# Optimization experiments

Hardware: AMD Instinct MI355X
Metric: run time of the kernel (lower is better)

## Reference

```python
import jax, jax.numpy as jnp
import numpy as np

N = 100000
E = 1600000
IN_C = 128
HID = 128
EMB = 64
EPS = 1e-5


def setup_inputs() -> dict:
    key = jax.random.key(0)
    ks = jax.random.split(key, 8)
    x = jax.random.normal(ks[0], (N, IN_C), dtype=jnp.float32)
    edge_index = jax.random.randint(ks[1], (2, E), 0, N, dtype=jnp.int64)
    s1 = 1.0 / np.sqrt(IN_C)
    s2 = 1.0 / np.sqrt(HID)
    # SAGEConv layer 1: lin_l (aggregated neighbors, with bias), lin_r (root, no bias)
    W1l = jax.random.uniform(ks[2], (IN_C, HID), jnp.float32, -s1, s1)
    b1 = jnp.zeros((HID,), jnp.float32)
    W1r = jax.random.uniform(ks[3], (IN_C, HID), jnp.float32, -s1, s1)
    g1 = jnp.ones((HID,), jnp.float32)
    be1 = jnp.zeros((HID,), jnp.float32)
    # SAGEConv layer 2
    W2l = jax.random.uniform(ks[4], (HID, EMB), jnp.float32, -s2, s2)
    b2 = jnp.zeros((EMB,), jnp.float32)
    W2r = jax.random.uniform(ks[5], (HID, EMB), jnp.float32, -s2, s2)
    g2 = jnp.ones((EMB,), jnp.float32)
    be2 = jnp.zeros((EMB,), jnp.float32)
    return {"x": x, "edge_index": edge_index,
            "W1l": W1l, "b1": b1, "W1r": W1r, "g1": g1, "be1": be1,
            "W2l": W2l, "b2": b2, "W2r": W2r, "g2": g2, "be2": be2}


def _mean_aggregate(x, src, dst, n_nodes):
    # mean of source-node features over incoming edges at each dst node
    msg_sum = jax.ops.segment_sum(x[src], dst, num_segments=n_nodes)  # [N, C]
    cnt = jax.ops.segment_sum(jnp.ones((src.shape[0],), x.dtype), dst,
                              num_segments=n_nodes)
    return msg_sum / jnp.maximum(cnt, 1.0)[:, None]


def _sage_conv(x, src, dst, Wl, b, Wr):
    agg = _mean_aggregate(x, src, dst, x.shape[0])
    return agg @ Wl + b + x @ Wr


def _batch_norm_eval(x, gamma, beta):
    # eval-mode BN with running_mean=0, running_var=1
    return x * (gamma / jnp.sqrt(1.0 + EPS)) + beta


def reference(x, edge_index, W1l, b1, W1r, g1, be1, W2l, b2, W2r, g2, be2):
    src, dst = edge_index[0], edge_index[1]
    h = _sage_conv(x, src, dst, W1l, b1, W1r)
    h = jax.nn.relu(_batch_norm_eval(h, g1, be1))  # dropout is identity in eval
    h = _sage_conv(h, src, dst, W2l, b2, W2r)
    h = jax.nn.relu(_batch_norm_eval(h, g2, be2))
    return h
```

## Files before the change

kernel.cpp:

```cpp
#include <hip/hip_runtime.h>
#include <math.h>

#define EPS 1e-5f
#define BSH 9
#define BSPAN 512
#define CHUNK 2048
#define CAP 16384

typedef __attribute__((ext_vector_type(8))) short short8;
typedef __attribute__((ext_vector_type(4))) float f32x4;

__device__ __forceinline__ short f2bf(float f) {
  union { float f; unsigned u; } v; v.f = f;
  unsigned r = v.u + 0x7fff + ((v.u >> 16) & 1);
  return (short)(r >> 16);
}
__device__ __forceinline__ float bf2f(unsigned short u) {
  union { unsigned u; float f; } v; v.u = ((unsigned)u) << 16; return v.f;
}

__global__ __launch_bounds__(256) void k_prep(
    const float* __restrict__ x, unsigned short* __restrict__ xbf, long long n8,
    const int* __restrict__ ei, int* __restrict__ bcnt, int E, int n,
    int ncast, int nhist,
    const float* __restrict__ W1l, const float* __restrict__ W1r,
    short* __restrict__ wp1,
    const float* __restrict__ W2l, const float* __restrict__ W2r,
    short* __restrict__ wp2) {
  __shared__ int h[256];
  int b = blockIdx.x, tid = threadIdx.x;
  if (b < ncast) {
    long long i = (long long)b * 256 + tid;
    if (i < n8) {
      const float4* p = (const float4*)x + i * 2;
      float4 v0 = p[0], v1 = p[1];
      short8 o;
      o[0] = f2bf(v0.x); o[1] = f2bf(v0.y); o[2] = f2bf(v0.z); o[3] = f2bf(v0.w);
      o[4] = f2bf(v1.x); o[5] = f2bf(v1.y); o[6] = f2bf(v1.z); o[7] = f2bf(v1.w);
      ((short8*)xbf)[i] = o;
    }
  } else if (b < ncast + nhist) {
    h[tid] = 0;
    __syncthreads();
    long long base = (long long)(b - ncast) * CHUNK;
#pragma unroll
    for (int i = 0; i < CHUNK / 256; ++i) {
      long long e = base + i * 256 + tid;
      if (e < E) {
        int d = ei[E + e];
        if ((unsigned)d < (unsigned)n) atomicAdd(&h[d >> BSH], 1);
      }
    }
    __syncthreads();
    if (h[tid]) atomicAdd(&bcnt[tid], h[tid]);
  } else if (b < ncast + nhist + 16) {
    int t = (b - ncast - nhist) * 256 + tid;
    int l = t & 63, f = t >> 6;
    int kt = f >> 3, ct = f & 7;
    int c = ct * 16 + (l & 15);
    int kb = kt * 32 + (l >> 4) * 8;
    short8 v;
#pragma unroll
    for (int j = 0; j < 8; ++j) {
      int k = kb + j;
      float w = (k < 128) ? W1l[k * 128 + c] : W1r[(k - 128) * 128 + c];
      v[j] = f2bf(w);
    }
    *(short8*)(wp1 + (size_t)t * 8) = v;
  } else {
    int t = (b - ncast - nhist - 16) * 256 + tid;
    int l = t & 63, f = t >> 6;
    int kt = f >> 3, ct = f & 7;
    int c = ct * 16 + (l & 15);
    int kb = kt * 32 + (l >> 4) * 8;
    short8 v;
#pragma unroll
    for (int j = 0; j < 8; ++j) {
      int k = kb + j;
      float w = (c < 64) ? W2l[k * 64 + c] : W2r[k * 64 + (c - 64)];
      v[j] = f2bf(w);
    }
    *(short8*)(wp2 + (size_t)t * 8) = v;
  }
}

__global__ __launch_bounds__(256) void k_bscan(
    const int* __restrict__ bcnt, int* __restrict__ bbase,
    int* __restrict__ bcur, int nbk) {
  __shared__ int s[256];
  int t = threadIdx.x;
  int v = (t < nbk) ? bcnt[t] : 0;
  s[t] = v;
  __syncthreads();
  for (int off = 1; off < 256; off <<= 1) {
    int xv = (t >= off) ? s[t - off] : 0;
    __syncthreads();
    s[t] += xv;
    __syncthreads();
  }
  int excl = s[t] - v;
  if (t < nbk) { bbase[t] = excl; bcur[t] = excl; }
}

__global__ __launch_bounds__(256) void k_scatter(
    const int* __restrict__ ei, int* __restrict__ bcur,
    unsigned* __restrict__ epk, int E, int n) {
  __shared__ int h[256];
  __shared__ int base[256];
  int tid = threadIdx.x;
  h[tid] = 0;
  __syncthreads();
  long long cbase = (long long)blockIdx.x * CHUNK;
  int src[CHUNK / 256], dl[CHUNK / 256], rk[CHUNK / 256], bk[CHUNK / 256];
#pragma unroll
  for (int i = 0; i < CHUNK / 256; ++i) {
    long long e = cbase + i * 256 + tid;
    bk[i] = -1;
    if (e < E) {
      int s = ei[e], d = ei[E + e];
      if ((unsigned)d < (unsigned)n) {
        bk[i] = d >> BSH; dl[i] = d & (BSPAN - 1); src[i] = s;
        rk[i] = atomicAdd(&h[bk[i]], 1);
      }
    }
  }
  __syncthreads();
  base[tid] = h[tid] ? atomicAdd(&bcur[tid], h[tid]) : 0;
  __syncthreads();
#pragma unroll
  for (int i = 0; i < CHUNK / 256; ++i) {
    if (bk[i] >= 0)
      epk[base[bk[i]] + rk[i]] = ((unsigned)dl[i] << 18) | (unsigned)src[i];
  }
}

__global__ __launch_bounds__(256) void k_build(
    const unsigned* __restrict__ epk, const int* __restrict__ bbase,
    const int* __restrict__ bcnt, int* __restrict__ rowptr,
    int* __restrict__ ssrc, int n, int nbk) {
  __shared__ int cnt[BSPAN];
  __shared__ int rp[BSPAN];
  __shared__ int cur[BSPAN];
  __shared__ int lsrc[CAP];
  int b = blockIdx.x, t = threadIdx.x;
  int segbase = bbase[b], segcnt = bcnt[b];
  int i0 = t, i1 = t + 256;
  cnt[i0] = 0; cnt[i1] = 0;
  __syncthreads();
  for (int i = t; i < segcnt; i += 256)
    atomicAdd(&cnt[epk[segbase + i] >> 18], 1);
  __syncthreads();
  rp[i0] = cnt[i0]; rp[i1] = cnt[i1];
  __syncthreads();
  for (int off = 1; off < BSPAN; off <<= 1) {
    int v0 = (i0 >= off) ? rp[i0 - off] : 0;
    int v1 = (i1 >= off) ? rp[i1 - off] : 0;
    __syncthreads();
    rp[i0] += v0; rp[i1] += v1;
    __syncthreads();
  }
  int e0 = rp[i0] - cnt[i0], e1 = rp[i1] - cnt[i1];
  cur[i0] = e0; cur[i1] = e1;
  int node0 = b * BSPAN;
  if (node0 + i0 < n) rowptr[node0 + i0] = segbase + e0;
  if (node0 + i1 < n) rowptr[node0 + i1] = segbase + e1;
  if (b == nbk - 1 && t == 0) rowptr[n] = segbase + segcnt;
  __syncthreads();
  if (segcnt <= CAP) {
    for (int i = t; i < segcnt; i += 256) {
      unsigned k = epk[segbase + i];
      int pos = atomicAdd(&cur[k >> 18], 1);
      lsrc[pos] = (int)(k & 0x3FFFFu);
    }
    __syncthreads();
    for (int i = t; i < segcnt; i += 256) ssrc[segbase + i] = lsrc[i];
  } else {
    for (int i = t; i < segcnt; i += 256) {
      unsigned k = epk[segbase + i];
      int pos = atomicAdd(&cur[k >> 18], 1);
      ssrc[segbase + pos] = (int)(k & 0x3FFFFu);
    }
  }
}

__global__ __launch_bounds__(256) void k_agg1(
    const int* __restrict__ rowptr, const int* __restrict__ ssrc,
    const unsigned* __restrict__ xbu, unsigned* __restrict__ aggu, int n) {
  int w = (blockIdx.x * 256 + threadIdx.x) >> 6;
  if (w >= n) return;
  int l = threadIdx.x & 63;
  int lh = l & 31;
  int hh = l >> 5;
  int beg = rowptr[w], end = rowptr[w + 1];
  float a0 = 0.f, a1 = 0.f, a2 = 0.f, a3 = 0.f;
  const uint2* xb2 = (const uint2*)xbu;
  int p = beg + hh;
  for (; p + 6 < end; p += 8) {
    int s0 = ssrc[p], s1 = ssrc[p + 2], s2 = ssrc[p + 4], s3 = ssrc[p + 6];
    uint2 v0 = xb2[(size_t)s0 * 32 + lh];
    uint2 v1 = xb2[(size_t)s1 * 32 + lh];
    uint2 v2 = xb2[(size_t)s2 * 32 + lh];
    uint2 v3 = xb2[(size_t)s3 * 32 + lh];
    a0 += bf2f((unsigned short)v0.x) + bf2f((unsigned short)v1.x)
        + bf2f((unsigned short)v2.x) + bf2f((unsigned short)v3.x);
    a1 += bf2f((unsigned short)(v0.x >> 16)) + bf2f((unsigned short)(v1.x >> 16))
        + bf2f((unsigned short)(v2.x >> 16)) + bf2f((unsigned short)(v3.x >> 16));
    a2 += bf2f((unsigned short)v0.y) + bf2f((unsigned short)v1.y)
        + bf2f((unsigned short)v2.y) + bf2f((unsigned short)v3.y);
    a3 += bf2f((unsigned short)(v0.y >> 16)) + bf2f((unsigned short)(v1.y >> 16))
        + bf2f((unsigned short)(v2.y >> 16)) + bf2f((unsigned short)(v3.y >> 16));
  }
  for (; p < end; p += 2) {
    uint2 v = xb2[(size_t)ssrc[p] * 32 + lh];
    a0 += bf2f((unsigned short)v.x);
    a1 += bf2f((unsigned short)(v.x >> 16));
    a2 += bf2f((unsigned short)v.y);
    a3 += bf2f((unsigned short)(v.y >> 16));
  }
  a0 += __shfl_xor(a0, 32, 64);
  a1 += __shfl_xor(a1, 32, 64);
  a2 += __shfl_xor(a2, 32, 64);
  a3 += __shfl_xor(a3, 32, 64);
  if (hh == 0) {
    float inv = 1.0f / fmaxf((float)(end - beg), 1.0f);
    unsigned o0 = ((unsigned)(unsigned short)f2bf(a1 * inv) << 16)
                | (unsigned short)f2bf(a0 * inv);
    unsigned o1 = ((unsigned)(unsigned short)f2bf(a3 * inv) << 16)
                | (unsigned short)f2bf(a2 * inv);
    ((uint2*)aggu)[(size_t)w * 32 + lh] = make_uint2(o0, o1);
  }
}

__global__ __launch_bounds__(256) void k_lin1(
    const unsigned short* __restrict__ xbf,
    const unsigned short* __restrict__ aggbf,
    const short* __restrict__ wp, const float* __restrict__ b,
    const float* __restrict__ g, const float* __restrict__ be,
    unsigned short* __restrict__ h1bf, int n) {
  __shared__ short As[64 * 256];
  int tid = threadIdx.x;
  int row0 = blockIdx.x * 64;
#pragma unroll
  for (int it = 0; it < 8; ++it) {
    int slot = it * 256 + tid;
    int r = slot >> 5;
    int c16 = slot & 31;
    int gr = row0 + r;
    short8 o = {0, 0, 0, 0, 0, 0, 0, 0};
    if (gr < n) {
      const unsigned short* src = (c16 < 16)
          ? (aggbf + (size_t)gr * 128 + c16 * 8)
          : (xbf + (size_t)gr * 128 + (c16 - 16) * 8);
      o = *(const short8*)src;
    }
    int byte = r * 512 + ((c16 * 16) ^ ((r & 7) << 4));
    *(short8*)((char*)As + byte) = o;
  }
  __syncthreads();
  int w = tid >> 6, l = tid & 63;
  int rloc = w * 16 + (l & 15);
  f32x4 acc[8];
#pragma unroll
  for (int i = 0; i < 8; ++i) acc[i] = (f32x4){0.f, 0.f, 0.f, 0.f};
#pragma unroll
  for (int kt = 0; kt < 8; ++kt) {
    int abyte = rloc * 512 + ((kt * 64 + (l >> 4) * 16) ^ ((rloc & 7) << 4));
    short8 a = *(short8*)((char*)As + abyte);
#pragma unroll
    for (int ct = 0; ct < 8; ++ct) {
      short8 bf = *(const short8*)(wp + ((size_t)((kt * 8 + ct) * 64 + l)) * 8);
      acc[ct] = __builtin_amdgcn_mfma_f32_16x16x32_bf16(a, bf, acc[ct], 0, 0, 0);
    }
  }
  int rbase = row0 + w * 16 + (l >> 4) * 4;
  int cb = l & 15;
#pragma unroll
  for (int ct = 0; ct < 8; ++ct) {
    int c = ct * 16 + cb;
    float sc = g[c] * (1.0f / sqrtf(1.0f + EPS));
    float bb = b[c], bt = be[c];
#pragma unroll
    for (int q = 0; q < 4; ++q) {
      int r = rbase + q;
      if (r < n) {
        float v = (acc[ct][q] + bb) * sc + bt;
        h1bf[(size_t)r * 128 + c] = (unsigned short)f2bf(fmaxf(v, 0.f));
      }
    }
  }
}

__global__ __launch_bounds__(256) void k_lin2(
    const unsigned short* __restrict__ h1bf, const short* __restrict__ wp,
    const float* __restrict__ b2,
    unsigned short* __restrict__ ybf, float* __restrict__ pre, int n) {
  __shared__ short As[64 * 128];
  int tid = threadIdx.x;
  int row0 = blockIdx.x * 64;
#pragma unroll
  for (int it = 0; it < 4; ++it) {
    int slot = it * 256 + tid;
    int r = slot >> 4;
    int c16 = slot & 15;
    int gr = row0 + r;
    short8 o = {0, 0, 0, 0, 0, 0, 0, 0};
    if (gr < n) o = *(const short8*)(h1bf + (size_t)gr * 128 + c16 * 8);
    int byte = r * 256 + ((c16 * 16) ^ ((r & 7) << 4));
    *(short8*)((char*)As + byte) = o;
  }
  __syncthreads();
  int w = tid >> 6, l = tid & 63;
  int rloc = w * 16 + (l & 15);
  f32x4 acc[8];
#pragma unroll
  for (int i = 0; i < 8; ++i) acc[i] = (f32x4){0.f, 0.f, 0.f, 0.f};
#pragma unroll
  for (int kt = 0; kt < 4; ++kt) {
    int abyte = rloc * 256 + ((kt * 64 + (l >> 4) * 16) ^ ((rloc & 7) << 4));
    short8 a = *(short8*)((char*)As + abyte);
#pragma unroll
    for (int ct = 0; ct < 8; ++ct) {
      short8 bf = *(const short8*)(wp + ((size_t)((kt * 8 + ct) * 64 + l)) * 8);
      acc[ct] = __builtin_amdgcn_mfma_f32_16x16x32_bf16(a, bf, acc[ct], 0, 0, 0);
    }
  }
  int rbase = row0 + w * 16 + (l >> 4) * 4;
  int cb = l & 15;
#pragma unroll
  for (int ct = 0; ct < 8; ++ct) {
    int c = ct * 16 + cb;
#pragma unroll
    for (int q = 0; q < 4; ++q) {
      int r = rbase + q;
      if (r < n) {
        if (c < 64) ybf[(size_t)r * 64 + c] = (unsigned short)f2bf(acc[ct][q]);
        else        pre[(size_t)r * 64 + (c - 64)] = acc[ct][q] + b2[c - 64];
      }
    }
  }
}

__global__ __launch_bounds__(256) void k_agg2(
    const int* __restrict__ rowptr, const int* __restrict__ ssrc,
    const unsigned* __restrict__ ybu, const float* __restrict__ g,
    const float* __restrict__ be, float* __restrict__ out, int n) {
  int w = (blockIdx.x * 256 + threadIdx.x) >> 6;
  if (w >= n) return;
  int l = threadIdx.x & 63;
  int lh = l & 31;
  int hh = l >> 5;
  int beg = rowptr[w], end = rowptr[w + 1];
  float a0 = 0.f, a1 = 0.f;
  int p = beg + hh;
  for (; p + 6 < end; p += 8) {
    int s0 = ssrc[p], s1 = ssrc[p + 2], s2 = ssrc[p + 4], s3 = ssrc[p + 6];
    unsigned v0 = ybu[(size_t)s0 * 32 + lh];
    unsigned v1 = ybu[(size_t)s1 * 32 + lh];
    unsigned v2 = ybu[(size_t)s2 * 32 + lh];
    unsigned v3 = ybu[(size_t)s3 * 32 + lh];
    a0 += bf2f((unsigned short)v0) + bf2f((unsigned short)v1)
        + bf2f((unsigned short)v2) + bf2f((unsigned short)v3);
    a1 += bf2f((unsigned short)(v0 >> 16)) + bf2f((unsigned short)(v1 >> 16))
        + bf2f((unsigned short)(v2 >> 16)) + bf2f((unsigned short)(v3 >> 16));
  }
  for (; p < end; p += 2) {
    unsigned v = ybu[(size_t)ssrc[p] * 32 + lh];
    a0 += bf2f((unsigned short)v);
    a1 += bf2f((unsigned short)(v >> 16));
  }
  a0 += __shfl_xor(a0, 32, 64);
  a1 += __shfl_xor(a1, 32, 64);
  if (hh == 0) {
    float inv = 1.0f / fmaxf((float)(end - beg), 1.0f);
    float r = 1.0f / sqrtf(1.0f + EPS);
    float2 g2 = ((const float2*)g)[lh];
    float2 be2 = ((const float2*)be)[lh];
    float2 po = ((float2*)out)[(size_t)w * 32 + lh];
    float v0 = (a0 * inv + po.x) * (g2.x * r) + be2.x;
    float v1 = (a1 * inv + po.y) * (g2.y * r) + be2.y;
    ((float2*)out)[(size_t)w * 32 + lh] = make_float2(fmaxf(v0, 0.f), fmaxf(v1, 0.f));
  }
}

extern "C" void kernel_launch(void* const* d_in, const int* in_sizes, int n_in,
                              void* d_out, int out_size, void* d_ws, size_t ws_size,
                              hipStream_t stream) {
  const float* x   = (const float*)d_in[0];
  const int*   ei  = (const int*)d_in[1];
  const float* W1l = (const float*)d_in[2];
  const float* b1  = (const float*)d_in[3];
  const float* W1r = (const float*)d_in[4];
  const float* g1  = (const float*)d_in[5];
  const float* be1 = (const float*)d_in[6];
  const float* W2l = (const float*)d_in[7];
  const float* b2  = (const float*)d_in[8];
  const float* W2r = (const float*)d_in[9];
  const float* g2  = (const float*)d_in[10];
  const float* be2 = (const float*)d_in[11];
  float* out = (float*)d_out;

  int n = in_sizes[0] / 128;
  int E = in_sizes[1] / 2;
  int nbk = (n + BSPAN - 1) / BSPAN;
  int nce = (int)(((long long)E + CHUNK - 1) / CHUNK);
  long long n8 = (long long)n * 16;
  int ncast = (int)((n8 + 255) / 256);

  char* ws = (char*)d_ws;
  size_t o = 0;
  auto carve = [&](size_t bytes) {
    char* p = ws + o;
    o += (bytes + 255) & ~(size_t)255;
    return p;
  };
  int*      bcnt   = (int*)carve(256 * 4);
  int*      bbase  = (int*)carve(256 * 4);
  int*      bcur   = (int*)carve(256 * 4);
  unsigned* epk    = (unsigned*)carve((size_t)E * 4);
  int*      ssrc   = (int*)carve((size_t)E * 4);
  int*      rowptr = (int*)carve((size_t)(n + 1) * 4);
  short*    wp1    = (short*)carve((size_t)64 * 64 * 8 * 2);
  short*    wp2    = (short*)carve((size_t)32 * 64 * 8 * 2);
  unsigned short* xbf   = (unsigned short*)carve((size_t)n * 128 * 2);
  unsigned short* aggbf = (unsigned short*)carve((size_t)n * 128 * 2);
  unsigned short* h1bf  = (unsigned short*)carve((size_t)n * 128 * 2);
  unsigned short* ybf   = (unsigned short*)carve((size_t)n * 64 * 2);

  hipMemsetAsync(bcnt, 0, 256 * 4, stream);

  k_prep<<<ncast + nce + 24, 256, 0, stream>>>(
      x, xbf, n8, ei, bcnt, E, n, ncast, nce,
      W1l, W1r, wp1, W2l, W2r, wp2);
  k_bscan<<<1, 256, 0, stream>>>(bcnt, bbase, bcur, nbk);
  k_scatter<<<nce, 256, 0, stream>>>(ei, bcur, epk, E, n);
  k_build<<<nbk, 256, 0, stream>>>(epk, bbase, bcnt, rowptr, ssrc, n, nbk);

  {
    long long T = (long long)n * 64;
    k_agg1<<<(int)((T + 255) / 256), 256, 0, stream>>>(
        rowptr, ssrc, (const unsigned*)xbf, (unsigned*)aggbf, n);
  }
  k_lin1<<<(n + 63) / 64, 256, 0, stream>>>(xbf, aggbf, wp1, b1, g1, be1, h1bf, n);
  k_lin2<<<(n + 63) / 64, 256, 0, stream>>>(h1bf, wp2, b2, ybf, out, n);
  {
    long long T = (long long)n * 64;
    k_agg2<<<(int)((T + 255) / 256), 256, 0, stream>>>(
        rowptr, ssrc, (const unsigned*)ybf, g2, be2, out, n);
  }
}
```

Before: 251.2 us.

## Fuse layer-1 neighbor aggregation into the MFMA linear kernel via shared memory

Merges the first-layer mean aggregation into the layer-1 GEMM kernel. Each wave gathers neighbor rows for its 16 rows and writes the bf16 means directly into the LDS A tile, which removes the aggbf global round-trip and one kernel launch. Both gather loops now use 4 edge lanes with wider 16-byte (layer 1) or 8-byte (layer 2) vector loads per lane, and layer 2 writes its epilogue as float4. The cost is lower gather parallelism per block: with 64 rows per block and serial per-row loops, this may hurt occupancy and latency hiding compared with one wave per node.

Measured after the change: 268.9 us. 1.07x slower.

```diff
diff --git a/kernel.cpp b/kernel.cpp
--- a/kernel.cpp
+++ b/kernel.cpp
@@ -183,81 +183,94 @@
   }
 }
 
-__global__ __launch_bounds__(256) void k_agg1(
+__global__ __launch_bounds__(256) void k_fused(
     const int* __restrict__ rowptr, const int* __restrict__ ssrc,
-    const unsigned* __restrict__ xbu, unsigned* __restrict__ aggu, int n) {
-  int w = (blockIdx.x * 256 + threadIdx.x) >> 6;
-  if (w >= n) return;
-  int l = threadIdx.x & 63;
-  int lh = l & 31;
-  int hh = l >> 5;
-  int beg = rowptr[w], end = rowptr[w + 1];
-  float a0 = 0.f, a1 = 0.f, a2 = 0.f, a3 = 0.f;
-  const uint2* xb2 = (const uint2*)xbu;
-  int p = beg + hh;
-  for (; p + 6 < end; p += 8) {
-    int s0 = ssrc[p], s1 = ssrc[p + 2], s2 = ssrc[p + 4], s3 = ssrc[p + 6];
-    uint2 v0 = xb2[(size_t)s0 * 32 + lh];
-    uint2 v1 = xb2[(size_t)s1 * 32 + lh];
-    uint2 v2 = xb2[(size_t)s2 * 32 + lh];
-    uint2 v3 = xb2[(size_t)s3 * 32 + lh];
-    a0 += bf2f((unsigned short)v0.x) + bf2f((unsigned short)v1.x)
-        + bf2f((unsigned short)v2.x) + bf2f((unsigned short)v3.x);
-    a1 += bf2f((unsigned short)(v0.x >> 16)) + bf2f((unsigned short)(v1.x >> 16))
-        + bf2f((unsigned short)(v2.x >> 16)) + bf2f((unsigned short)(v3.x >> 16));
-    a2 += bf2f((unsigned short)v0.y) + bf2f((unsigned short)v1.y)
-        + bf2f((unsigned short)v2.y) + bf2f((unsigned short)v3.y);
-    a3 += bf2f((unsigned short)(v0.y >> 16)) + bf2f((unsigned short)(v1.y >> 16))
-        + bf2f((unsigned short)(v2.y >> 16)) + bf2f((unsigned short)(v3.y >> 16));
-  }
-  for (; p < end; p += 2) {
-    uint2 v = xb2[(size_t)ssrc[p] * 32 + lh];
-    a0 += bf2f((unsigned short)v.x);
-    a1 += bf2f((unsigned short)(v.x >> 16));
-    a2 += bf2f((unsigned short)v.y);
-    a3 += bf2f((unsigned short)(v.y >> 16));
-  }
-  a0 += __shfl_xor(a0, 32, 64);
-  a1 += __shfl_xor(a1, 32, 64);
-  a2 += __shfl_xor(a2, 32, 64);
-  a3 += __shfl_xor(a3, 32, 64);
-  if (hh == 0) {
-    float inv = 1.0f / fmaxf((float)(end - beg), 1.0f);
-    unsigned o0 = ((unsigned)(unsigned short)f2bf(a1 * inv) << 16)
-                | (unsigned short)f2bf(a0 * inv);
-    unsigned o1 = ((unsigned)(unsigned short)f2bf(a3 * inv) << 16)
-                | (unsigned short)f2bf(a2 * inv);
-    ((uint2*)aggu)[(size_t)w * 32 + lh] = make_uint2(o0, o1);
-  }
-}
-
-__global__ __launch_bounds__(256) void k_lin1(
     const unsigned short* __restrict__ xbf,
-    const unsigned short* __restrict__ aggbf,
     const short* __restrict__ wp, const float* __restrict__ b,
     const float* __restrict__ g, const float* __restrict__ be,
     unsigned short* __restrict__ h1bf, int n) {
   __shared__ short As[64 * 256];
   int tid = threadIdx.x;
   int row0 = blockIdx.x * 64;
-#pragma unroll
-  for (int it = 0; it < 8; ++it) {
+  int w = tid >> 6, l = tid & 63;
+  int q = l >> 4, ql = l & 15;
+
+#pragma unroll
+  for (int it = 0; it < 4; ++it) {
     int slot = it * 256 + tid;
-    int r = slot >> 5;
-    int c16 = slot & 31;
+    int r = slot >> 4;
+    int c16 = 16 + (slot & 15);
     int gr = row0 + r;
     short8 o = {0, 0, 0, 0, 0, 0, 0, 0};
-    if (gr < n) {
-      const unsigned short* src = (c16 < 16)
-          ? (aggbf + (size_t)gr * 128 + c16 * 8)
-          : (xbf + (size_t)gr * 128 + (c16 - 16) * 8);
-      o = *(const short8*)src;
-    }
+    if (gr < n) o = *(const short8*)(xbf + (size_t)gr * 128 + (slot & 15) * 8);
     int byte = r * 512 + ((c16 * 16) ^ ((r & 7) << 4));
     *(short8*)((char*)As + byte) = o;
   }
-  __syncthreads();
-  int w = tid >> 6, l = tid & 63;
+
+  const uint4* xb4 = (const uint4*)xbf;
+  for (int i = 0; i < 16; ++i) {
+    int r = w * 16 + i;
+    int gr = row0 + r;
+    float a[8] = {0.f, 0.f, 0.f, 0.f, 0.f, 0.f, 0.f, 0.f};
+    int beg = 0, end = 0;
+    if (gr < n) { beg = rowptr[gr]; end = rowptr[gr + 1]; }
+    int p = beg + q;
+    for (; p + 12 < end; p += 16) {
+      int s0 = ssrc[p], s1 = ssrc[p + 4], s2 = ssrc[p + 8], s3 = ssrc[p + 12];
+      uint4 v0 = xb4[(size_t)s0 * 16 + ql];
+      uint4 v1 = xb4[(size_t)s1 * 16 + ql];
+      uint4 v2 = xb4[(size_t)s2 * 16 + ql];
+      uint4 v3 = xb4[(size_t)s3 * 16 + ql];
+      a[0] += bf2f((unsigned short)v0.x) + bf2f((unsigned short)v1.x)
+            + bf2f((unsigned short)v2.x) + bf2f((unsigned short)v3.x);
+      a[1] += bf2f((unsigned short)(v0.x >> 16)) + bf2f((unsigned short)(v1.x >> 16))
+            + bf2f((unsigned short)(v2.x >> 16)) + bf2f((unsigned short)(v3.x >> 16));
+      a[2] += bf2f((unsigned short)v0.y) + bf2f((unsigned short)v1.y)
+            + bf2f((unsigned short)v2.y) + bf2f((unsigned short)v3.y);
+      a[3] += bf2f((unsigned short)(v0.y >> 16)) + bf2f((unsigned short)(v1.y >> 16))
+            + bf2f((unsigned short)(v2.y >> 16)) + bf2f((unsigned short)(v3.y >> 16));
+      a[4] += bf2f((unsigned short)v0.z) + bf2f((unsigned short)v1.z)
+            + bf2f((unsigned short)v2.z) + bf2f((unsigned short)v3.z);
+      a[5] += bf2f((unsigned short)(v0.z >> 16)) + bf2f((unsigned short)(v1.z >> 16))
+            + bf2f((unsigned short)(v2.z >> 16)) + bf2f((unsigned short)(v3.z >> 16));
+      a[6] += bf2f((unsigned short)v0.w) + bf2f((unsigned short)v1.w)
+            + bf2f((unsigned short)v2.w) + bf2f((unsigned short)v3.w);
+      a[7] += bf2f((unsigned short)(v0.w >> 16)) + bf2f((unsigned short)(v1.w >> 16))
+            + bf2f((unsigned short)(v2.w >> 16)) + bf2f((unsigned short)(v3.w >> 16));
+    }
+    for (; p < end; p += 4) {
+      uint4 v = xb4[(size_t)ssrc[p] * 16 + ql];
+      a[0] += bf2f((unsigned short)v.x);
+      a[1] += bf2f((unsigned short)(v.x >> 16));
+      a[2] += bf2f((unsigned short)v.y);
+      a[3] += bf2f((unsigned short)(v.y >> 16));
+      a[4] += bf2f((unsigned short)v.z);
+      a[5] += bf2f((unsigned short)(v.z >> 16));
+      a[6] += bf2f((unsigned short)v.w);
+      a[7] += bf2f((unsigned short)(v.w >> 16));
+    }
+#pragma unroll
+    for (int j = 0; j < 8; ++j) {
+      a[j] += __shfl_xor(a[j], 16, 64);
+      a[j] += __shfl_xor(a[j], 32, 64);
+    }
+    if (q == 0) {
+      float inv = 1.0f / fmaxf((float)(end - beg), 1.0f);
+      uint4 o;
+      o.x = ((unsigned)(unsigned short)f2bf(a[1] * inv) << 16)
+          | (unsigned short)f2bf(a[0] * inv);
+      o.y = ((unsigned)(unsigned short)f2bf(a[3] * inv) << 16)
+          | (unsigned short)f2bf(a[2] * inv);
+      o.z = ((unsigned)(unsigned short)f2bf(a[5] * inv) << 16)
+          | (unsigned short)f2bf(a[4] * inv);
+      o.w = ((unsigned)(unsigned short)f2bf(a[7] * inv) << 16)
+          | (unsigned short)f2bf(a[6] * inv);
+      int byte = r * 512 + ((ql * 16) ^ ((r & 7) << 4));
+      *(uint4*)((char*)As + byte) = o;
+    }
+  }
+  __syncthreads();
+
   int rloc = w * 16 + (l & 15);
   f32x4 acc[8];
 #pragma unroll
@@ -265,11 +278,11 @@
 #pragma unroll
   for (int kt = 0; kt < 8; ++kt) {
     int abyte = rloc * 512 + ((kt * 64 + (l >> 4) * 16) ^ ((rloc & 7) << 4));
-    short8 a = *(short8*)((char*)As + abyte);
+    short8 af = *(short8*)((char*)As + abyte);
 #pragma unroll
     for (int ct = 0; ct < 8; ++ct) {
       short8 bf = *(const short8*)(wp + ((size_t)((kt * 8 + ct) * 64 + l)) * 8);
-      acc[ct] = __builtin_amdgcn_mfma_f32_16x16x32_bf16(a, bf, acc[ct], 0, 0, 0);
+      acc[ct] = __builtin_amdgcn_mfma_f32_16x16x32_bf16(af, bf, acc[ct], 0, 0, 0);
     }
   }
   int rbase = row0 + w * 16 + (l >> 4) * 4;
@@ -280,10 +293,10 @@
     float sc = g[c] * (1.0f / sqrtf(1.0f + EPS));
     float bb = b[c], bt = be[c];
 #pragma unroll
-    for (int q = 0; q < 4; ++q) {
-      int r = rbase + q;
+    for (int qq = 0; qq < 4; ++qq) {
+      int r = rbase + qq;
       if (r < n) {
-        float v = (acc[ct][q] + bb) * sc + bt;
+        float v = (acc[ct][qq] + bb) * sc + bt;
         h1bf[(size_t)r * 128 + c] = (unsigned short)f2bf(fmaxf(v, 0.f));
       }
     }
@@ -347,38 +360,49 @@
   int w = (blockIdx.x * 256 + threadIdx.x) >> 6;
   if (w >= n) return;
   int l = threadIdx.x & 63;
-  int lh = l & 31;
-  int hh = l >> 5;
+  int q = l >> 4, ql = l & 15;
   int beg = rowptr[w], end = rowptr[w + 1];
-  float a0 = 0.f, a1 = 0.f;
-  int p = beg + hh;
-  for (; p + 6 < end; p += 8) {
-    int s0 = ssrc[p], s1 = ssrc[p + 2], s2 = ssrc[p + 4], s3 = ssrc[p + 6];
-    unsigned v0 = ybu[(size_t)s0 * 32 + lh];
-    unsigned v1 = ybu[(size_t)s1 * 32 + lh];
-    unsigned v2 = ybu[(size_t)s2 * 32 + lh];
-    unsigned v3 = ybu[(size_t)s3 * 32 + lh];
-    a0 += bf2f((unsigned short)v0) + bf2f((unsigned short)v1)
-        + bf2f((unsigned short)v2) + bf2f((unsigned short)v3);
-    a1 += bf2f((unsigned short)(v0 >> 16)) + bf2f((unsigned short)(v1 >> 16))
-        + bf2f((unsigned short)(v2 >> 16)) + bf2f((unsigned short)(v3 >> 16));
-  }
-  for (; p < end; p += 2) {
-    unsigned v = ybu[(size_t)ssrc[p] * 32 + lh];
-    a0 += bf2f((unsigned short)v);
-    a1 += bf2f((unsigned short)(v >> 16));
-  }
-  a0 += __shfl_xor(a0, 32, 64);
-  a1 += __shfl_xor(a1, 32, 64);
-  if (hh == 0) {
+  float a0 = 0.f, a1 = 0.f, a2 = 0.f, a3 = 0.f;
+  const uint2* yb2 = (const uint2*)ybu;
+  int p = beg + q;
+  for (; p + 12 < end; p += 16) {
+    int s0 = ssrc[p], s1 = ssrc[p + 4], s2 = ssrc[p + 8], s3 = ssrc[p + 12];
+    uint2 v0 = yb2[(size_t)s0 * 16 + ql];
+    uint2 v1 = yb2[(size_t)s1 * 16 + ql];
+    uint2 v2 = yb2[(size_t)s2 * 16 + ql];
+    uint2 v3 = yb2[(size_t)s3 * 16 + ql];
+    a0 += bf2f((unsigned short)v0.x) + bf2f((unsigned short)v1.x)
+        + bf2f((unsigned short)v2.x) + bf2f((unsigned short)v3.x);
+    a1 += bf2f((unsigned short)(v0.x >> 16)) + bf2f((unsigned short)(v1.x >> 16))
+        + bf2f((unsigned short)(v2.x >> 16)) + bf2f((unsigned short)(v3.x >> 16));
+    a2 += bf2f((unsigned short)v0.y) + bf2f((unsigned short)v1.y)
+        + bf2f((unsigned short)v2.y) + bf2f((unsigned short)v3.y);
+    a3 += bf2f((unsigned short)(v0.y >> 16)) + bf2f((unsigned short)(v1.y >> 16))
+        + bf2f((unsigned short)(v2.y >> 16)) + bf2f((unsigned short)(v3.y >> 16));
+  }
+  for (; p < end; p += 4) {
+    uint2 v = yb2[(size_t)ssrc[p] * 16 + ql];
+    a0 += bf2f((unsigned short)v.x);
+    a1 += bf2f((unsigned short)(v.x >> 16));
+    a2 += bf2f((unsigned short)v.y);
+    a3 += bf2f((unsigned short)(v.y >> 16));
+  }
+  a0 += __shfl_xor(a0, 16, 64); a0 += __shfl_xor(a0, 32, 64);
+  a1 += __shfl_xor(a1, 16, 64); a1 += __shfl_xor(a1, 32, 64);
+  a2 += __shfl_xor(a2, 16, 64); a2 += __shfl_xor(a2, 32, 64);
+  a3 += __shfl_xor(a3, 16, 64); a3 += __shfl_xor(a3, 32, 64);
+  if (q == 0) {
     float inv = 1.0f / fmaxf((float)(end - beg), 1.0f);
-    float r = 1.0f / sqrtf(1.0f + EPS);
-    float2 g2 = ((const float2*)g)[lh];
-    float2 be2 = ((const float2*)be)[lh];
-    float2 po = ((float2*)out)[(size_t)w * 32 + lh];
-    float v0 = (a0 * inv + po.x) * (g2.x * r) + be2.x;
-    float v1 = (a1 * inv + po.y) * (g2.y * r) + be2.y;
-    ((float2*)out)[(size_t)w * 32 + lh] = make_float2(fmaxf(v0, 0.f), fmaxf(v1, 0.f));
+    float rr = 1.0f / sqrtf(1.0f + EPS);
+    float4 gv = ((const float4*)g)[ql];
+    float4 bv = ((const float4*)be)[ql];
+    float4 po = ((const float4*)out)[(size_t)w * 16 + ql];
+    float4 v;
+    v.x = fmaxf((a0 * inv + po.x) * (gv.x * rr) + bv.x, 0.f);
+    v.y = fmaxf((a1 * inv + po.y) * (gv.y * rr) + bv.y, 0.f);
+    v.z = fmaxf((a2 * inv + po.z) * (gv.z * rr) + bv.z, 0.f);
+    v.w = fmaxf((a3 * inv + po.w) * (gv.w * rr) + bv.w, 0.f);
+    ((float4*)out)[(size_t)w * 16 + ql] = v;
   }
 }
 
@@ -422,7 +446,6 @@
   short*    wp1    = (short*)carve((size_t)64 * 64 * 8 * 2);
   short*    wp2    = (short*)carve((size_t)32 * 64 * 8 * 2);
   unsigned short* xbf   = (unsigned short*)carve((size_t)n * 128 * 2);
-  unsigned short* aggbf = (unsigned short*)carve((size_t)n * 128 * 2);
   unsigned short* h1bf  = (unsigned short*)carve((size_t)n * 128 * 2);
   unsigned short* ybf   = (unsigned short*)carve((size_t)n * 64 * 2);
 
@@ -435,12 +458,8 @@
   k_scatter<<<nce, 256, 0, stream>>>(ei, bcur, epk, E, n);
   k_build<<<nbk, 256, 0, stream>>>(epk, bbase, bcnt, rowptr, ssrc, n, nbk);
 
-  {
-    long long T = (long long)n * 64;
-    k_agg1<<<(int)((T + 255) / 256), 256, 0, stream>>>(
-        rowptr, ssrc, (const unsigned*)xbf, (unsigned*)aggbf, n);
-  }
-  k_lin1<<<(n + 63) / 64, 256, 0, stream>>>(xbf, aggbf, wp1, b1, g1, be1, h1bf, n);
+  k_fused<<<(n + 63) / 64, 256, 0, stream>>>(
+      rowptr, ssrc, xbf, wp1, b1, g1, be1, h1bf, n);
   k_lin2<<<(n + 63) / 64, 256, 0, stream>>>(h1bf, wp2, b2, ybf, out, n);
   {
     long long T = (long long)n * 64;
```
